# Optimization experiments

Measured on AMD Instinct MI355X. Metric: run time of the kernel, lower is better.

Reference implementation:

```python
import jax, jax.numpy as jnp
import numpy as np

D_MODEL = 768
D_STATE = 8
EXPAND = 2
D_HEAD = 64
D_CONV = 4
D_INNER = EXPAND * D_MODEL            # 1536
N_HEADS = D_INNER // D_HEAD           # 24
PARAM_DIM = 2                         # (A_freq, dt) per head per step
D_PROJ = 2 * D_INNER + N_HEADS * PARAM_DIM  # 3120
D_FF = 4 * D_MODEL
BATCH, SEQ = 2, 2048


def setup_inputs() -> dict:
    key = jax.random.key(0)
    ks = jax.random.split(key, 8)
    def s(k, shape, scale):
        return jax.random.normal(k, shape, dtype=jnp.float32) * scale
    return {
        "x": s(ks[0], (BATCH, SEQ, D_MODEL), 1.0),
        "norm1_w": jnp.ones((D_MODEL,), jnp.float32),
        "w_in": s(ks[1], (D_MODEL, D_PROJ), D_MODEL ** -0.5),
        "conv_w": s(ks[2], (D_INNER, D_CONV), D_CONV ** -0.5),
        "w_bc": s(ks[3], (D_INNER, 2 * N_HEADS * D_STATE), D_INNER ** -0.5),
        "D_skip": s(ks[4], (N_HEADS,), 1.0),
        "w_out": s(ks[5], (D_INNER, D_MODEL), D_INNER ** -0.5),
        "norm2_w": jnp.ones((D_MODEL,), jnp.float32),
        "ff_w1": s(ks[6], (D_MODEL, D_FF), D_MODEL ** -0.5),
        "ff_b1": jnp.zeros((D_FF,), jnp.float32),
        "ff_w2": s(ks[7], (D_FF, D_MODEL), D_FF ** -0.5),
        "ff_b2": jnp.zeros((D_MODEL,), jnp.float32),
    }


def _rmsnorm(x, w, eps=1e-6):
    return x * jax.lax.rsqrt(jnp.mean(x * x, axis=-1, keepdims=True) + eps) * w


def _l2norm(x, eps=1e-12):
    # normalize_bc=True: L2-normalize B/C rows over the state dim
    return x * jax.lax.rsqrt(jnp.sum(x * x, axis=-1, keepdims=True) + eps)


def _mixer(x, w_in, conv_w, w_bc, D_skip, w_out):
    Bsz, T, _ = x.shape
    proj = x @ w_in  # (B,T,3120)
    gate, vraw, params = jnp.split(proj, [D_INNER, 2 * D_INNER], axis=-1)
    # causal depthwise conv over time
    vpad = jnp.pad(vraw, ((0, 0), (D_CONV - 1, 0), (0, 0)))
    kernel = conv_w.T[:, None, :]  # (K, 1, C) for WIO, groups=C
    conv = jax.lax.conv_general_dilated(
        vpad, kernel, window_strides=(1,), padding='VALID',
        dimension_numbers=('NWC', 'WIO', 'NWC'), feature_group_count=D_INNER)
    v = jax.nn.silu(conv)  # (B,T,D_INNER)
    # B/C projections per head (normalized rows)
    bc = (v @ w_bc).reshape(Bsz, T, N_HEADS, 2, D_STATE)
    Bm = _l2norm(bc[..., 0, :])  # (B,T,H,N)
    Cm = _l2norm(bc[..., 1, :])  # (B,T,H,N)
    # LinOSS-IM discretizer: per-head time-varying frequency A and step dt
    p = params.reshape(Bsz, T, N_HEADS, PARAM_DIM)
    A = jax.nn.softplus(p[..., 0])
    dt = jax.nn.sigmoid(p[..., 1])
    S = 1.0 / (1.0 + dt * dt * A)  # implicit-midpoint Schur factor
    u = v.reshape(Bsz, T, N_HEADS, D_HEAD)
    tfirst = lambda a: jnp.moveaxis(a, 1, 0)

    def step(carry, inp):
        z, xs = carry  # each (B,H,N,P): velocity / position of the oscillator
        Bt, Ct, At, dtt, St, ut = inp
        d = dtt[..., None, None]
        a = At[..., None, None]
        s = St[..., None, None]
        bu = Bt[..., :, None] * ut[..., None, :]  # (B,H,N,P)
        z = s * (z - d * a * xs + d * bu)
        xs = xs + d * z
        y = jnp.einsum('bhn,bhnp->bhp', Ct, xs)
        return (z, xs), y

    z0 = jnp.zeros((Bsz, N_HEADS, D_STATE, D_HEAD), x.dtype)
    _, ys = jax.lax.scan(step, (z0, z0),
                         (tfirst(Bm), tfirst(Cm), tfirst(A), tfirst(dt), tfirst(S), tfirst(u)))
    y = jnp.moveaxis(ys, 0, 1)  # (B,T,H,P)
    # gate + per-head skip (D * u), then out projection
    gated = (y + D_skip[None, None, :, None] * u) * jax.nn.silu(gate).reshape(Bsz, T, N_HEADS, D_HEAD)
    return gated.reshape(Bsz, T, D_INNER) @ w_out


def reference(x, norm1_w, w_in, conv_w, w_bc, D_skip, w_out, norm2_w, ff_w1, ff_b1, ff_w2, ff_b2):
    x = x + _mixer(_rmsnorm(x, norm1_w), w_in, conv_w, w_bc, D_skip, w_out)
    h = _rmsnorm(x, norm2_w)
    return x + (jax.nn.gelu(h @ ff_w1 + ff_b1) @ ff_w2 + ff_b2)
```

## Files before the change

### kernel.cpp

```cpp
#include <hip/hip_runtime.h>

#define DMODEL 768
#define DINNER 1536
#define NHEADS 24
#define DHEAD  64
#define DSTATE 8
#define DPROJ  3120
#define DFF    3072
#define BATCH  2
#define SEQ    2048
#define BTTOT  (BATCH*SEQ)
#define NCHUNK 64
#define CT     32
#define NTBLK  8688

typedef unsigned short u16;
typedef __attribute__((ext_vector_type(8))) short bf16x8;
typedef __attribute__((ext_vector_type(4))) float f32x4;

__device__ __forceinline__ float b2f(u16 u){
  union { unsigned u; float f; } x; x.u = ((unsigned)u) << 16; return x.f;
}
__device__ __forceinline__ u16 f2b(float f){
  union { float f; unsigned u; } x; x.f = f;
  unsigned r = x.u + 0x7FFF + ((x.u >> 16) & 1);
  return (u16)(r >> 16);
}
__device__ __forceinline__ float ldin(const void* p, size_t i, bool f32){
  return f32 ? ((const float*)p)[i] : b2f(((const u16*)p)[i]);
}
__device__ __forceinline__ bool wire_f32(const u16* probe){ return probe[0] == 0; }

struct TDesc { const void* src; u16* dst; int R, C, bx, blk0; };
struct TPack { TDesc d[5]; };

__global__ __launch_bounds__(256) void pre_k(
    TPack P, const void* __restrict__ x, const void* __restrict__ w,
    u16* __restrict__ xn, const u16* __restrict__ probe)
{
  const bool f32 = wire_f32(probe);
  int bk = blockIdx.x;
  if (bk >= NTBLK){
    const size_t row = bk - NTBLK;
    float v[3]; float s = 0.f;
    #pragma unroll
    for (int i = 0; i < 3; i++){
      size_t idx = row * DMODEL + threadIdx.x + 256 * i;
      float f = ldin(x, idx, f32);
      v[i] = f; s += f * f;
    }
    #pragma unroll
    for (int o = 32; o > 0; o >>= 1) s += __shfl_xor(s, o);
    __shared__ float red[4];
    if ((threadIdx.x & 63) == 0) red[threadIdx.x >> 6] = s;
    __syncthreads();
    float tot = red[0] + red[1] + red[2] + red[3];
    float inv = rsqrtf(tot * (1.0f / DMODEL) + 1e-6f);
    #pragma unroll
    for (int i = 0; i < 3; i++){
      int c = threadIdx.x + 256 * i;
      xn[row * DMODEL + c] = f2b(v[i] * inv * ldin(w, c, f32));
    }
    return;
  }
  int s = 0;
  #pragma unroll
  for (int i = 1; i < 5; i++) if (bk >= P.d[i].blk0) s = i;
  const TDesc D = P.d[s];
  const int local = bk - D.blk0;
  const int cx = local % D.bx, ry = local / D.bx;
  const int c0 = cx * 32, r0 = ry * 32;
  const int R = D.R, C = D.C;
  __shared__ u16 tile[32][33];
  const int tx = threadIdx.x & 31, ty = threadIdx.x >> 5;
  #pragma unroll
  for (int i = 0; i < 32; i += 8){
    int r = r0 + ty + i, c = c0 + tx;
    u16 val = 0;
    if (r < R && c < C){
      size_t idx = (size_t)r * C + c;
      val = f32 ? f2b(((const float*)D.src)[idx]) : ((const u16*)D.src)[idx];
    }
    tile[ty + i][tx] = val;
  }
  __syncthreads();
  #pragma unroll
  for (int i = 0; i < 32; i += 8){
    int c = c0 + ty + i, r = r0 + tx;
    if (c < C && r < R) D.dst[(size_t)c * R + r] = tile[tx][ty + i];
  }
}

__global__ __launch_bounds__(256) void rmsnormW_k(
    const u16* __restrict__ pW, const void* __restrict__ x, const void* __restrict__ w,
    float* __restrict__ x2, u16* __restrict__ out, const u16* __restrict__ probe)
{
  const bool f32 = wire_f32(probe);
  const size_t row = blockIdx.x;
  const size_t MN = (size_t)BTTOT * DMODEL;
  float v[3]; float s = 0.f;
  #pragma unroll
  for (int i = 0; i < 3; i++){
    size_t idx = row * DMODEL + threadIdx.x + 256 * i;
    float f = ldin(x, idx, f32) + b2f(pW[idx]) + b2f(pW[MN + idx])
            + b2f(pW[2 * MN + idx]) + b2f(pW[3 * MN + idx]);
    x2[idx] = f;
    v[i] = f; s += f * f;
  }
  #pragma unroll
  for (int o = 32; o > 0; o >>= 1) s += __shfl_xor(s, o);
  __shared__ float red[4];
  if ((threadIdx.x & 63) == 0) red[threadIdx.x >> 6] = s;
  __syncthreads();
  float tot = red[0] + red[1] + red[2] + red[3];
  float inv = rsqrtf(tot * (1.0f / DMODEL) + 1e-6f);
  #pragma unroll
  for (int i = 0; i < 3; i++){
    int c = threadIdx.x + 256 * i;
    out[row * DMODEL + c] = f2b(v[i] * inv * ldin(w, c, f32));
  }
}

template <class Epi>
__global__ __launch_bounds__(256, 2) void gemm_bt(
    const u16* __restrict__ A, const u16* __restrict__ Bt,
    int M, int N, int Ks, int ldK, Epi epi, const u16* __restrict__ probe)
{
  const bool wf32 = wire_f32(probe);
  __shared__ __align__(16) u16 As[128 * 64];
  __shared__ __align__(16) u16 Bs[128 * 64];
  const int tid  = threadIdx.x;
  const int lane = tid & 63;
  const int wave = tid >> 6;
  const int wm = (wave >> 1) * 64;
  const int wn = (wave & 1) * 64;
  const int m0 = blockIdx.y * 128;
  const int n0 = blockIdx.x * 128;
  const int z  = blockIdx.z;
  const int kbase = z * Ks;
  const int rt = tid >> 3;
  const int cb = (tid & 7) * 8;
  const int sw = (rt & 7) * 8;

  f32x4 acc[4][4];
  const f32x4 z4 = {0.f, 0.f, 0.f, 0.f};
  #pragma unroll
  for (int i = 0; i < 4; i++)
    #pragma unroll
    for (int j = 0; j < 4; j++) acc[i][j] = z4;

  const int krow = lane & 15;
  const int kqo  = (lane >> 4) * 8;
  const int rsw  = (krow & 7) * 8;

  for (int k0 = kbase; k0 < kbase + Ks; k0 += 64){
    __syncthreads();
    #pragma unroll
    for (int i = 0; i < 4; i++){
      const u16* ga = A + ((size_t)(m0 + rt + 32 * i) * ldK + k0 + (cb ^ sw));
      __builtin_amdgcn_global_load_lds(
          (const __attribute__((address_space(1))) unsigned*)ga,
          (__attribute__((address_space(3))) unsigned*)(As + i * 2048 + wave * 512),
          16, 0, 0);
      int rb = n0 + rt + 32 * i; if (rb > N - 1) rb = N - 1;
      const u16* gb = Bt + ((size_t)rb * ldK + k0 + (cb ^ sw));
      __builtin_amdgcn_global_load_lds(
          (const __attribute__((address_space(1))) unsigned*)gb,
          (__attribute__((address_space(3))) unsigned*)(Bs + i * 2048 + wave * 512),
          16, 0, 0);
    }
    __syncthreads();
    #pragma unroll
    for (int ks = 0; ks < 2; ks++){
      const int koff = (ks * 32 + kqo) ^ rsw;
      bf16x8 af[4], bfr[4];
      #pragma unroll
      for (int i = 0; i < 4; i++){
        af[i]  = *(const bf16x8*)(As + (wm + i * 16 + krow) * 64 + koff);
        bfr[i] = *(const bf16x8*)(Bs + (wn + i * 16 + krow) * 64 + koff);
      }
      #pragma unroll
      for (int i = 0; i < 4; i++)
        #pragma unroll
        for (int j = 0; j < 4; j++)
          acc[i][j] = __builtin_amdgcn_mfma_f32_16x16x32_bf16(af[i], bfr[j], acc[i][j], 0, 0, 0);
    }
  }

  const int mb = m0 + wm + (lane >> 4) * 4;
  const int nb = n0 + wn + (lane & 15);
  #pragma unroll
  for (int i = 0; i < 4; i++)
    #pragma unroll
    for (int j = 0; j < 4; j++)
      #pragma unroll
      for (int r = 0; r < 4; r++){
        int m = mb + i * 16 + r;
        int n = nb + j * 16;
        if (n < N) epi(acc[i][j][r], m, n, wf32, z);
      }
}

struct EpiBf16 {
  u16* out; int ldo;
  __device__ void operator()(float v, int m, int n, bool, int) const {
    out[(size_t)m * ldo + n] = f2b(v);
  }
};
struct EpiPartB {
  u16* out; size_t ss; int ldo;
  __device__ void operator()(float v, int m, int n, bool, int z) const {
    out[(size_t)z * ss + (size_t)m * ldo + n] = f2b(v);
  }
};
struct EpiBiasGelu {
  u16* out; const void* bias; int ldo;
  __device__ void operator()(float v, int m, int n, bool f32, int) const {
    float x = v + ldin(bias, n, f32);
    float t = 0.7978845608028654f * (x + 0.044715f * x * x * x);
    out[(size_t)m * ldo + n] = f2b(0.5f * x * (1.0f + tanhf(t)));
  }
};

__global__ __launch_bounds__(256) void reduceF_k(
    const u16* __restrict__ pF, const void* __restrict__ bias,
    const float* __restrict__ x2, void* __restrict__ out,
    const u16* __restrict__ probe)
{
  const bool f32 = wire_f32(probe);
  const size_t MN = (size_t)BTTOT * DMODEL;
  size_t i = ((size_t)blockIdx.x * 256 + threadIdx.x) * 4;
  int n = (int)(i % DMODEL);
  float4 r = *(const float4*)(x2 + i);
  float o[4] = {r.x, r.y, r.z, r.w};
  #pragma unroll
  for (int k = 0; k < 4; k++){
    ushort4 p = *(const ushort4*)(pF + k * MN + i);
    o[0] += b2f(p.x); o[1] += b2f(p.y); o[2] += b2f(p.z); o[3] += b2f(p.w);
  }
  #pragma unroll
  for (int j = 0; j < 4; j++) o[j] += ldin(bias, n + j, f32);
  if (f32){
    *(float4*)((float*)out + i) = make_float4(o[0], o[1], o[2], o[3]);
  } else {
    u16* po = (u16*)out + i;
    po[0] = f2b(o[0]); po[1] = f2b(o[1]); po[2] = f2b(o[2]); po[3] = f2b(o[3]);
  }
}

__global__ __launch_bounds__(256) void conv_silu_k(
    const u16* __restrict__ proj, const void* __restrict__ cw, u16* __restrict__ v,
    const u16* __restrict__ probe)
{
  const bool f32 = wire_f32(probe);
  const int strip = blockIdx.x / 6;
  const int c = (blockIdx.x % 6) * 256 + threadIdx.x;
  const int bt0 = strip * 32;
  const bool head = (bt0 & (SEQ - 1)) == 0;
  const u16* base = proj + (size_t)bt0 * DPROJ + DINNER + c;
  const float w0 = ldin(cw, c * 4 + 0, f32), w1 = ldin(cw, c * 4 + 1, f32);
  const float w2 = ldin(cw, c * 4 + 2, f32), w3 = ldin(cw, c * 4 + 3, f32);
  float s0 = head ? 0.f : b2f(base[-3 * DPROJ]);
  float s1 = head ? 0.f : b2f(base[-2 * DPROJ]);
  float s2 = head ? 0.f : b2f(base[-1 * DPROJ]);
  u16* ov = v + (size_t)bt0 * DINNER + c;
  #pragma unroll
  for (int t = 0; t < 32; t++){
    float s3 = b2f(base[(size_t)t * DPROJ]);
    float a = fmaf(w0, s0, fmaf(w1, s1, fmaf(w2, s2, w3 * s3)));
    ov[(size_t)t * DINNER] = f2b(a / (1.f + __expf(-a)));
    s0 = s1; s1 = s2; s2 = s3;
  }
}

__global__ __launch_bounds__(256) void prep_k(
    const u16* __restrict__ proj, const u16* __restrict__ pB,
    float* __restrict__ bcn, float* __restrict__ prm)
{
  const size_t MNb = (size_t)BTTOT * 2 * NHEADS * DSTATE;
  int idx = blockIdx.x * 256 + threadIdx.x;
  if (idx >= BTTOT * NHEADS) return;
  int h = idx % NHEADS; int bt = idx / NHEADS;
  int b = bt >> 11, t = bt & (SEQ - 1);
  float p0 = b2f(proj[(size_t)bt * DPROJ + 2 * DINNER + h * 2]);
  float p1 = b2f(proj[(size_t)bt * DPROJ + 2 * DINNER + h * 2 + 1]);
  float A  = fmaxf(p0, 0.f) + log1pf(__expf(-fabsf(p0)));
  float dt = 1.f / (1.f + __expf(-p1));
  float S  = 1.f / (1.f + dt * dt * A);
  size_t pb = ((size_t)(b * NHEADS + h) * SEQ + t);
  float* pr = prm + pb * 4;
  pr[0] = S * dt * A; pr[1] = dt; pr[2] = S * dt; pr[3] = S;
  const u16* br = pB + (size_t)bt * (2 * NHEADS * DSTATE) + h * 16;
  float Bv[8] = {0,0,0,0,0,0,0,0}, Cv[8] = {0,0,0,0,0,0,0,0};
  #pragma unroll
  for (int k = 0; k < 8; k++){
    ushort4 b0 = *(const ushort4*)(br + k * MNb);
    ushort4 b1 = *(const ushort4*)(br + k * MNb + 4);
    ushort4 c0 = *(const ushort4*)(br + k * MNb + 8);
    ushort4 c1 = *(const ushort4*)(br + k * MNb + 12);
    Bv[0] += b2f(b0.x); Bv[1] += b2f(b0.y); Bv[2] += b2f(b0.z); Bv[3] += b2f(b0.w);
    Bv[4] += b2f(b1.x); Bv[5] += b2f(b1.y); Bv[6] += b2f(b1.z); Bv[7] += b2f(b1.w);
    Cv[0] += b2f(c0.x); Cv[1] += b2f(c0.y); Cv[2] += b2f(c0.z); Cv[3] += b2f(c0.w);
    Cv[4] += b2f(c1.x); Cv[5] += b2f(c1.y); Cv[6] += b2f(c1.z); Cv[7] += b2f(c1.w);
  }
  float sB = 1e-12f, sC = 1e-12f;
  #pragma unroll
  for (int j = 0; j < 8; j++){ sB += Bv[j] * Bv[j]; sC += Cv[j] * Cv[j]; }
  float rB = rsqrtf(sB), rC = rsqrtf(sC);
  float* o = bcn + pb * 16;
  #pragma unroll
  for (int j = 0; j < 8; j++){ o[j * 2] = Bv[j] * rB; o[j * 2 + 1] = Cv[j] * rC; }
}

__global__ __launch_bounds__(256) void scanA(
    const float* __restrict__ bcn, const float* __restrict__ prm,
    const u16* __restrict__ v, float2* __restrict__ rend, float4* __restrict__ phiE)
{
  if (blockIdx.x >= 768){
    int g = (blockIdx.x - 768) * 256 + threadIdx.x;
    if (g >= 48 * NCHUNK) return;
    const float4* pr = (const float4*)(prm + (size_t)g * CT * 4);
    float p00 = 1.f, p01 = 0.f, p10 = 0.f, p11 = 1.f;
    #pragma unroll 4
    for (int t = 0; t < CT; t++){
      float4 pv = pr[t];
      float n00 = pv.w * p00 - pv.x * p10;
      float n01 = pv.w * p01 - pv.x * p11;
      float n10 = fmaf(pv.z, p00, pv.w * p10);
      float n11 = fmaf(pv.z, p01, pv.w * p11);
      p00 = n00; p01 = n01; p10 = n10; p11 = n11;
    }
    phiE[g] = make_float4(p00, p01, p10, p11);
    return;
  }
  const int g = blockIdx.x * 4 + (threadIdx.x >> 6);
  const int bh = g >> 6, chunk = g & 63;
  const int b = bh / NHEADS, h = bh % NHEADS;
  const int t0 = chunk * CT;
  const int lane = threadIdx.x & 63;
  const float4* bcB = (const float4*)(bcn + ((size_t)bh * SEQ + t0) * 16);
  const float4* prB = (const float4*)(prm + ((size_t)bh * SEQ + t0) * 4);
  const u16* vB = v + ((size_t)b * SEQ + t0) * DINNER + h * DHEAD + lane;

  float z[8], xs[8];
  #pragma unroll
  for (int n = 0; n < 8; n++){ z[n] = 0.f; xs[n] = 0.f; }
  #pragma unroll 4
  for (int t = 0; t < CT; t++){
    float4 pv  = prB[t];
    float4 bc0 = bcB[t * 4 + 0], bc1 = bcB[t * 4 + 1];
    float4 bc2 = bcB[t * 4 + 2], bc3 = bcB[t * 4 + 3];
    float u = b2f(vB[(size_t)t * DINNER]);
    float Bv[8] = {bc0.x, bc0.z, bc1.x, bc1.z, bc2.x, bc2.z, bc3.x, bc3.z};
    #pragma unroll
    for (int n = 0; n < 8; n++){
      z[n]  = pv.w * z[n] - pv.x * xs[n] + pv.z * (Bv[n] * u);
      xs[n] = fmaf(pv.y, z[n], xs[n]);
    }
  }
  float2* rb = rend + (size_t)g * 512 + lane;
  #pragma unroll
  for (int n = 0; n < 8; n++) rb[n * 64] = make_float2(z[n], xs[n]);
}

__global__ __launch_bounds__(512) void scanB(
    const float2* __restrict__ rend, const float4* __restrict__ phiE,
    float2* __restrict__ s0)
{
  const int bh = blockIdx.x, tid = threadIdx.x;
  float z = 0.f, xs = 0.f;
  for (int c = 0; c < NCHUNK; c++){
    size_t idx = ((size_t)bh * NCHUNK + c) * 512 + tid;
    s0[idx] = make_float2(z, xs);
    float4 ph = phiE[bh * NCHUNK + c];
    float2 r  = rend[idx];
    float nz = ph.x * z + ph.y * xs + r.x;
    float nx = ph.z * z + ph.w * xs + r.y;
    z = nz; xs = nx;
  }
}

__global__ __launch_bounds__(256) void scanC(
    const float* __restrict__ bcn, const float* __restrict__ prm,
    const u16* __restrict__ v, const u16* __restrict__ proj,
    const float2* __restrict__ s0, const void* __restrict__ Dsk,
    u16* __restrict__ gated, const u16* __restrict__ probe)
{
  const bool f32 = wire_f32(probe);
  const int g = blockIdx.x * 4 + (threadIdx.x >> 6);
  const int bh = g >> 6, chunk = g & 63;
  const int b = bh / NHEADS, h = bh % NHEADS;
  const int t0 = chunk * CT;
  const int lane = threadIdx.x & 63;
  const float4* bcB = (const float4*)(bcn + ((size_t)bh * SEQ + t0) * 16);
  const float4* prB = (const float4*)(prm + ((size_t)bh * SEQ + t0) * 4);
  const u16* vB = v     + ((size_t)b * SEQ + t0) * DINNER + h * DHEAD + lane;
  const u16* gB = proj  + ((size_t)b * SEQ + t0) * DPROJ  + h * DHEAD + lane;
  u16*       oB = gated + ((size_t)b * SEQ + t0) * DINNER + h * DHEAD + lane;
  const float dsk = ldin(Dsk, h, f32);

  float z[8], xs[8];
  const float2* sb = s0 + (size_t)g * 512 + lane;
  #pragma unroll
  for (int n = 0; n < 8; n++){ float2 s = sb[n * 64]; z[n] = s.x; xs[n] = s.y; }
  #pragma unroll 4
  for (int t = 0; t < CT; t++){
    float4 pv  = prB[t];
    float4 bc0 = bcB[t * 4 + 0], bc1 = bcB[t * 4 + 1];
    float4 bc2 = bcB[t * 4 + 2], bc3 = bcB[t * 4 + 3];
    float u  = b2f(vB[(size_t)t * DINNER]);
    float gt = b2f(gB[(size_t)t * DPROJ]);
    float Bv[8] = {bc0.x, bc0.z, bc1.x, bc1.z, bc2.x, bc2.z, bc3.x, bc3.z};
    float Cv[8] = {bc0.y, bc0.w, bc1.y, bc1.w, bc2.y, bc2.w, bc3.y, bc3.w};
    float y = 0.f;
    #pragma unroll
    for (int n = 0; n < 8; n++){
      z[n]  = pv.w * z[n] - pv.x * xs[n] + pv.z * (Bv[n] * u);
      xs[n] = fmaf(pv.y, z[n], xs[n]);
      y     = fmaf(Cv[n], xs[n], y);
    }
    float sil = gt / (1.f + __expf(-gt));
    oB[(size_t)t * DINNER] = f2b((y + dsk * u) * sil);
  }
}

extern "C" void kernel_launch(void* const* d_in, const int* in_sizes, int n_in,
                              void* d_out, int out_size, void* d_ws, size_t ws_size,
                              hipStream_t stream)
{
  const void* x      = d_in[0];
  const u16*  probe  = (const u16*)d_in[1];
  const void* norm1w = d_in[1];
  const void* w_in   = d_in[2];
  const void* conv_w = d_in[3];
  const void* w_bc   = d_in[4];
  const void* Dsk    = d_in[5];
  const void* w_out  = d_in[6];
  const void* norm2w = d_in[7];
  const void* ff_w1  = d_in[8];
  const void* ff_b1  = d_in[9];
  const void* ff_w2  = d_in[10];
  const void* ff_b2  = d_in[11];

  char* wsb = (char*)d_ws;
  size_t off = 0;
  auto alloc = [&](size_t bytes) -> void* {
    void* p = wsb + off; off += (bytes + 255) & ~(size_t)255; return p;
  };
  u16*   w_inT  = (u16*)  alloc((size_t)DPROJ * DMODEL * 2);
  u16*   w_bcT  = (u16*)  alloc((size_t)(2 * NHEADS * DSTATE) * DINNER * 2);
  u16*   w_outT = (u16*)  alloc((size_t)DMODEL * DINNER * 2);
  u16*   ff_w1T = (u16*)  alloc((size_t)DFF * DMODEL * 2);
  u16*   ff_w2T = (u16*)  alloc((size_t)DMODEL * DFF * 2);
  u16*   xn     = (u16*)  alloc((size_t)BTTOT * DMODEL * 2);
  u16*   proj   = (u16*)  alloc((size_t)BTTOT * DPROJ * 2);
  u16*   v      = (u16*)  alloc((size_t)BTTOT * DINNER * 2);
  float* bcn    = (float*)alloc((size_t)48 * SEQ * 16 * 4);
  float* prm    = (float*)alloc((size_t)48 * SEQ * 4 * 4);
  u16*   gated  = (u16*)  alloc((size_t)BTTOT * DINNER * 2);
  float* x2     = (float*)alloc((size_t)BTTOT * DMODEL * 4);
  u16*   hbuf   = (u16*)  alloc((size_t)BTTOT * DMODEL * 2);
  float4* phiE  = (float4*)alloc((size_t)48 * NCHUNK * 16);
  char*  scrU   = (char*) alloc((size_t)27 * 1024 * 1024);
  u16*   pB     = (u16*)scrU;
  float2* rend  = (float2*)scrU;
  float2* s0b   = (float2*)(scrU + (size_t)48 * NCHUNK * 512 * 8);
  u16*   pF     = (u16*)scrU;
  u16*   pW     = proj;
  u16*   a1     = proj;

  TPack tp;
  tp.d[0] = {w_in,  w_inT,  DMODEL, DPROJ,               98, 0};
  tp.d[1] = {w_bc,  w_bcT,  DINNER, 2 * NHEADS * DSTATE, 12, 2352};
  tp.d[2] = {w_out, w_outT, DINNER, DMODEL,              24, 2928};
  tp.d[3] = {ff_w1, ff_w1T, DMODEL, DFF,                 96, 4080};
  tp.d[4] = {ff_w2, ff_w2T, DFF,    DMODEL,              24, 6384};
  pre_k<<<NTBLK + BTTOT, 256, 0, stream>>>(tp, x, norm1w, xn, probe);

  gemm_bt<<<dim3(25, 32, 1), 256, 0, stream>>>(xn, w_inT, BTTOT, DPROJ, DMODEL, DMODEL,
                                               EpiBf16{proj, DPROJ}, probe);
  conv_silu_k<<<768, 256, 0, stream>>>(proj, conv_w, v, probe);
  gemm_bt<<<dim3(3, 32, 8), 256, 0, stream>>>(v, w_bcT, BTTOT, 2 * NHEADS * DSTATE,
                                              1536 / 8, DINNER,
                                              EpiPartB{pB, (size_t)BTTOT * 2 * NHEADS * DSTATE, 2 * NHEADS * DSTATE}, probe);
  prep_k<<<(BTTOT * NHEADS) / 256, 256, 0, stream>>>(proj, pB, bcn, prm);

  scanA<<<780, 256, 0, stream>>>(bcn, prm, v, rend, phiE);
  scanB<<<48, 512, 0, stream>>>(rend, phiE, s0b);
  scanC<<<48 * NCHUNK / 4, 256, 0, stream>>>(bcn, prm, v, proj, s0b, Dsk, gated, probe);

  gemm_bt<<<dim3(6, 32, 4), 256, 0, stream>>>(gated, w_outT, BTTOT, DMODEL, 1536 / 4, DINNER,
                                              EpiPartB{pW, (size_t)BTTOT * DMODEL, DMODEL}, probe);
  rmsnormW_k<<<BTTOT, 256, 0, stream>>>(pW, x, norm2w, x2, hbuf, probe);
  gemm_bt<<<dim3(24, 32, 1), 256, 0, stream>>>(hbuf, ff_w1T, BTTOT, DFF, DMODEL, DMODEL,
                                               EpiBiasGelu{a1, ff_b1, DFF}, probe);
  gemm_bt<<<dim3(6, 32, 4), 256, 0, stream>>>(a1, ff_w2T, BTTOT, DMODEL, 3072 / 4, DFF,
                                              EpiPartB{pF, (size_t)BTTOT * DMODEL, DMODEL}, probe);
  reduceF_k<<<(BTTOT * DMODEL) / 1024, 256, 0, stream>>>(pF, ff_b2, x2, d_out, probe);
}
```

Baseline: 350.7 us.

## Fuse B/C normalization and param prep into chunked scan first pass

Removes the separate prep_k kernel. Each scanA wave now computes its chunk's discretization params and L2-normalized B/C rows into shared memory, writes them out for scanC, and runs the local scan from LDS. The per-chunk transition matrix product is folded into the same loop instead of extra blocks. Scratch buffers are split into two regions so pB and rend no longer alias. This saves a launch and a global round trip, at the cost of more work and LDS per scanA block.

```diff
diff --git a/kernel.cpp b/kernel.cpp
--- a/kernel.cpp
+++ b/kernel.cpp
@@ -273,83 +273,77 @@
   }
 }
 
-__global__ __launch_bounds__(256) void prep_k(
+__global__ __launch_bounds__(256) void scanA(
     const u16* __restrict__ proj, const u16* __restrict__ pB,
-    float* __restrict__ bcn, float* __restrict__ prm)
-{
-  const size_t MNb = (size_t)BTTOT * 2 * NHEADS * DSTATE;
-  int idx = blockIdx.x * 256 + threadIdx.x;
-  if (idx >= BTTOT * NHEADS) return;
-  int h = idx % NHEADS; int bt = idx / NHEADS;
-  int b = bt >> 11, t = bt & (SEQ - 1);
-  float p0 = b2f(proj[(size_t)bt * DPROJ + 2 * DINNER + h * 2]);
-  float p1 = b2f(proj[(size_t)bt * DPROJ + 2 * DINNER + h * 2 + 1]);
-  float A  = fmaxf(p0, 0.f) + log1pf(__expf(-fabsf(p0)));
-  float dt = 1.f / (1.f + __expf(-p1));
-  float S  = 1.f / (1.f + dt * dt * A);
-  size_t pb = ((size_t)(b * NHEADS + h) * SEQ + t);
-  float* pr = prm + pb * 4;
-  pr[0] = S * dt * A; pr[1] = dt; pr[2] = S * dt; pr[3] = S;
-  const u16* br = pB + (size_t)bt * (2 * NHEADS * DSTATE) + h * 16;
-  float Bv[8] = {0,0,0,0,0,0,0,0}, Cv[8] = {0,0,0,0,0,0,0,0};
-  #pragma unroll
-  for (int k = 0; k < 8; k++){
-    ushort4 b0 = *(const ushort4*)(br + k * MNb);
-    ushort4 b1 = *(const ushort4*)(br + k * MNb + 4);
-    ushort4 c0 = *(const ushort4*)(br + k * MNb + 8);
-    ushort4 c1 = *(const ushort4*)(br + k * MNb + 12);
-    Bv[0] += b2f(b0.x); Bv[1] += b2f(b0.y); Bv[2] += b2f(b0.z); Bv[3] += b2f(b0.w);
-    Bv[4] += b2f(b1.x); Bv[5] += b2f(b1.y); Bv[6] += b2f(b1.z); Bv[7] += b2f(b1.w);
-    Cv[0] += b2f(c0.x); Cv[1] += b2f(c0.y); Cv[2] += b2f(c0.z); Cv[3] += b2f(c0.w);
-    Cv[4] += b2f(c1.x); Cv[5] += b2f(c1.y); Cv[6] += b2f(c1.z); Cv[7] += b2f(c1.w);
-  }
-  float sB = 1e-12f, sC = 1e-12f;
-  #pragma unroll
-  for (int j = 0; j < 8; j++){ sB += Bv[j] * Bv[j]; sC += Cv[j] * Cv[j]; }
-  float rB = rsqrtf(sB), rC = rsqrtf(sC);
-  float* o = bcn + pb * 16;
-  #pragma unroll
-  for (int j = 0; j < 8; j++){ o[j * 2] = Bv[j] * rB; o[j * 2 + 1] = Cv[j] * rC; }
-}
-
-__global__ __launch_bounds__(256) void scanA(
-    const float* __restrict__ bcn, const float* __restrict__ prm,
-    const u16* __restrict__ v, float2* __restrict__ rend, float4* __restrict__ phiE)
-{
-  if (blockIdx.x >= 768){
-    int g = (blockIdx.x - 768) * 256 + threadIdx.x;
-    if (g >= 48 * NCHUNK) return;
-    const float4* pr = (const float4*)(prm + (size_t)g * CT * 4);
-    float p00 = 1.f, p01 = 0.f, p10 = 0.f, p11 = 1.f;
-    #pragma unroll 4
-    for (int t = 0; t < CT; t++){
-      float4 pv = pr[t];
-      float n00 = pv.w * p00 - pv.x * p10;
-      float n01 = pv.w * p01 - pv.x * p11;
-      float n10 = fmaf(pv.z, p00, pv.w * p10);
-      float n11 = fmaf(pv.z, p01, pv.w * p11);
-      p00 = n00; p01 = n01; p10 = n10; p11 = n11;
-    }
-    phiE[g] = make_float4(p00, p01, p10, p11);
-    return;
-  }
-  const int g = blockIdx.x * 4 + (threadIdx.x >> 6);
+    const u16* __restrict__ v, float* __restrict__ bcn, float* __restrict__ prm,
+    float2* __restrict__ rend, float4* __restrict__ phiE)
+{
+  const int wave = threadIdx.x >> 6;
+  const int lane = threadIdx.x & 63;
+  const int g = blockIdx.x * 4 + wave;
   const int bh = g >> 6, chunk = g & 63;
   const int b = bh / NHEADS, h = bh % NHEADS;
   const int t0 = chunk * CT;
-  const int lane = threadIdx.x & 63;
-  const float4* bcB = (const float4*)(bcn + ((size_t)bh * SEQ + t0) * 16);
-  const float4* prB = (const float4*)(prm + ((size_t)bh * SEQ + t0) * 4);
+
+  __shared__ float sbc[4][CT * 16];
+  __shared__ float spr[4][CT * 4];
+
+  {
+    const int t = lane >> 1, half = lane & 1;
+    const int bt = b * SEQ + t0 + t;
+    if (half == 0){
+      float p0 = b2f(proj[(size_t)bt * DPROJ + 2 * DINNER + h * 2]);
+      float p1 = b2f(proj[(size_t)bt * DPROJ + 2 * DINNER + h * 2 + 1]);
+      float A  = fmaxf(p0, 0.f) + log1pf(__expf(-fabsf(p0)));
+      float dt = 1.f / (1.f + __expf(-p1));
+      float S  = 1.f / (1.f + dt * dt * A);
+      spr[wave][t * 4 + 0] = S * dt * A;
+      spr[wave][t * 4 + 1] = dt;
+      spr[wave][t * 4 + 2] = S * dt;
+      spr[wave][t * 4 + 3] = S;
+    }
+    const size_t MNb = (size_t)BTTOT * 2 * NHEADS * DSTATE;
+    const u16* br = pB + (size_t)bt * (2 * NHEADS * DSTATE) + h * 16 + half * 8;
+    float vs[8] = {0,0,0,0,0,0,0,0};
+    #pragma unroll
+    for (int k = 0; k < 8; k++){
+      ushort4 a0 = *(const ushort4*)(br + k * MNb);
+      ushort4 a1 = *(const ushort4*)(br + k * MNb + 4);
+      vs[0] += b2f(a0.x); vs[1] += b2f(a0.y); vs[2] += b2f(a0.z); vs[3] += b2f(a0.w);
+      vs[4] += b2f(a1.x); vs[5] += b2f(a1.y); vs[6] += b2f(a1.z); vs[7] += b2f(a1.w);
+    }
+    float s = 1e-12f;
+    #pragma unroll
+    for (int j = 0; j < 8; j++) s += vs[j] * vs[j];
+    float r = rsqrtf(s);
+    #pragma unroll
+    for (int j = 0; j < 8; j++) sbc[wave][t * 16 + j * 2 + half] = vs[j] * r;
+  }
+  __syncthreads();
+
+  {
+    float4* gb = (float4*)(bcn + ((size_t)bh * SEQ + t0) * 16);
+    const float4* sb4 = (const float4*)sbc[wave];
+    gb[lane]      = sb4[lane];
+    gb[lane + 64] = sb4[lane + 64];
+    if (lane < 32){
+      float4* gp = (float4*)(prm + ((size_t)bh * SEQ + t0) * 4);
+      gp[lane] = ((const float4*)spr[wave])[lane];
+    }
+  }
+
   const u16* vB = v + ((size_t)b * SEQ + t0) * DINNER + h * DHEAD + lane;
-
   float z[8], xs[8];
   #pragma unroll
   for (int n = 0; n < 8; n++){ z[n] = 0.f; xs[n] = 0.f; }
+  float p00 = 1.f, p01 = 0.f, p10 = 0.f, p11 = 1.f;
   #pragma unroll 4
   for (int t = 0; t < CT; t++){
-    float4 pv  = prB[t];
-    float4 bc0 = bcB[t * 4 + 0], bc1 = bcB[t * 4 + 1];
-    float4 bc2 = bcB[t * 4 + 2], bc3 = bcB[t * 4 + 3];
+    float4 pv  = *(const float4*)&spr[wave][t * 4];
+    float4 bc0 = *(const float4*)&sbc[wave][t * 16 + 0];
+    float4 bc1 = *(const float4*)&sbc[wave][t * 16 + 4];
+    float4 bc2 = *(const float4*)&sbc[wave][t * 16 + 8];
+    float4 bc3 = *(const float4*)&sbc[wave][t * 16 + 12];
     float u = b2f(vB[(size_t)t * DINNER]);
     float Bv[8] = {bc0.x, bc0.z, bc1.x, bc1.z, bc2.x, bc2.z, bc3.x, bc3.z};
     #pragma unroll
@@ -357,10 +351,16 @@
       z[n]  = pv.w * z[n] - pv.x * xs[n] + pv.z * (Bv[n] * u);
       xs[n] = fmaf(pv.y, z[n], xs[n]);
     }
+    float n00 = pv.w * p00 - pv.x * p10;
+    float n01 = pv.w * p01 - pv.x * p11;
+    float n10 = fmaf(pv.z, p00, pv.w * p10);
+    float n11 = fmaf(pv.z, p01, pv.w * p11);
+    p00 = n00; p01 = n01; p10 = n10; p11 = n11;
   }
   float2* rb = rend + (size_t)g * 512 + lane;
   #pragma unroll
   for (int n = 0; n < 8; n++) rb[n * 64] = make_float2(z[n], xs[n]);
+  if (lane == 0) phiE[g] = make_float4(p00, p01, p10, p11);
 }
 
 __global__ __launch_bounds__(512) void scanB(
@@ -461,11 +461,12 @@
   float* x2     = (float*)alloc((size_t)BTTOT * DMODEL * 4);
   u16*   hbuf   = (u16*)  alloc((size_t)BTTOT * DMODEL * 2);
   float4* phiE  = (float4*)alloc((size_t)48 * NCHUNK * 16);
-  char*  scrU   = (char*) alloc((size_t)27 * 1024 * 1024);
-  u16*   pB     = (u16*)scrU;
-  float2* rend  = (float2*)scrU;
-  float2* s0b   = (float2*)(scrU + (size_t)48 * NCHUNK * 512 * 8);
-  u16*   pF     = (u16*)scrU;
+  char*  reg1   = (char*) alloc((size_t)26 * 1024 * 1024);
+  u16*   pB     = (u16*)reg1;
+  u16*   pF     = (u16*)reg1;
+  char*  reg2   = (char*) alloc((size_t)26 * 1024 * 1024);
+  float2* rend  = (float2*)reg2;
+  float2* s0b   = (float2*)(reg2 + (size_t)48 * NCHUNK * 512 * 8);
   u16*   pW     = proj;
   u16*   a1     = proj;
 
@@ -483,11 +484,10 @@
   gemm_bt<<<dim3(3, 32, 8), 256, 0, stream>>>(v, w_bcT, BTTOT, 2 * NHEADS * DSTATE,
                                               1536 / 8, DINNER,
                                               EpiPartB{pB, (size_t)BTTOT * 2 * NHEADS * DSTATE, 2 * NHEADS * DSTATE}, probe);
-  prep_k<<<(BTTOT * NHEADS) / 256, 256, 0, stream>>>(proj, pB, bcn, prm);
-
-  scanA<<<780, 256, 0, stream>>>(bcn, prm, v, rend, phiE);
+
+  scanA<<<768, 256, 0, stream>>>(proj, pB, v, bcn, prm, rend, phiE);
   scanB<<<48, 512, 0, stream>>>(rend, phiE, s0b);
-  scanC<<<48 * NCHUNK / 4, 256, 0, stream>>>(bcn, prm, v, proj, s0b, Dsk, gated, probe);
+  scanC<<<768, 256, 0, stream>>>(bcn, prm, v, proj, s0b, Dsk, gated, probe);
 
   gemm_bt<<<dim3(6, 32, 4), 256, 0, stream>>>(gated, w_outT, BTTOT, DMODEL, 1536 / 4, DINNER,
                                               EpiPartB{pW, (size_t)BTTOT * DMODEL, DMODEL}, probe);
```

Result: faster. 340.3 us (-3.0%).
